# Performance work log

Measured on AMD Instinct MI355X. Metric: run time of the kernel, lower is better.

## Reference

```python
import jax, jax.numpy as jnp
import numpy as np

ALPHA = 0.9
T = 809          # doc_len_limit hard-coded in fofe_tricontext_encoder
M = 16           # opt['max_len'] (cand_len_limit)
BN_EPS = 1e-5


def _cand_indices(T, M):
    # Enumeration order matches get_sample_index: outer over start s, inner over span.
    s_list, e_list = [], []
    for s in range(T):
        for span in range(min(M, T - s)):
            s_list.append(s)
            e_list.append(s + span)
    return np.asarray(s_list, np.int32), np.asarray(e_list, np.int32)

_S_IDX, _E_IDX = _cand_indices(T, M)          # [N_CANDS] = [12824]
_SPAN = (_E_IDX - _S_IDX).astype(np.int64)
# FOFE decay coefficient alpha^(e-s+1) for subtracting the prefix before the span
_COEF = (ALPHA ** (_SPAN + 1)).astype(np.float32)
# Lower-triangular FOFE prefix operator: A[t,k] = alpha^(t-k) for k<=t
_DIFF = np.subtract.outer(np.arange(T), np.arange(T))
_AFWD = np.where(_DIFF >= 0, ALPHA ** np.maximum(_DIFF, 0), 0.0).astype(np.float32)


def _bn(x, g, b, m, v):
    return (x - m) * jax.lax.rsqrt(v + BN_EPS) * g + b


def _forward(doc_emb, query_emb, W1, g1, b1, m1, v1, W2, g2, b2, m2, v2, W3):
    B, Tt, Dd = doc_emb.shape
    A = jnp.asarray(_AFWD)
    # forward FOFE prefixes F[t] = sum_{k<=t} alpha^(t-k) x[k]; inverse FOFE suffixes
    F = jnp.einsum('tk,bkd->btd', A, doc_emb)          # [B,T,Dd]
    R = jnp.einsum('tk,bkd->btd', A.T, doc_emb)        # [B,T,Dd]
    Fp = jnp.concatenate([jnp.zeros((B, 1, Dd), F.dtype), F], axis=1)   # Fp[:,s]=F[s-1]
    Rp = jnp.concatenate([R, jnp.zeros((B, 1, Dd), R.dtype)], axis=1)   # Rp[:,e+1]
    s_idx = jnp.asarray(_S_IDX)
    e_idx = jnp.asarray(_E_IDX)
    coef = jnp.asarray(_COEF)
    lctx = Fp[:, s_idx]                                 # left context excl cand
    cand = F[:, e_idx] - coef[None, :, None] * Fp[:, s_idx]  # FOFE of span [s,e]
    rctx = Rp[:, e_idx + 1]                             # right context excl cand
    doc_fofe = jnp.concatenate([lctx, cand, rctx], axis=-1)  # [B,N,3*Dd]
    # query FOFE (fofe_linear): z = sum_t alpha^(Lq-1-t) q[t]
    Lq = query_emb.shape[1]
    w = (ALPHA ** jnp.arange(Lq - 1, -1, -1, dtype=jnp.float32))
    qf = jnp.einsum('t,btd->bd', w, query_emb)          # [B,E]
    N = doc_fofe.shape[1]
    qf_b = jnp.broadcast_to(qf[:, None, :], (B, N, qf.shape[-1]))
    dq = jnp.concatenate([doc_fofe, qf_b], axis=-1)     # [B,N,3*Dd+E]
    x = dq.reshape(B * N, -1)
    h = jax.nn.relu(_bn(x @ W1.T, g1, b1, m1, v1))      # 1x1 conv == GEMM
    h = jax.nn.relu(_bn(h @ W2.T, g2, b2, m2, v2))
    out = (h @ W3.T).reshape(B, N, 2)                   # 2 class scores per candidate
    return out


def setup_inputs() -> dict:
    key = jax.random.key(0)
    ks = jax.random.split(key, 13)
    B, Lq, Dd, E = 4, 30, 304, 300
    Cin, H4, H2 = 3 * Dd + E, 1024, 512
    return {
        'doc_emb': jax.random.normal(ks[0], (B, T, Dd), jnp.float32),
        'query_emb': jax.random.normal(ks[1], (B, Lq, E), jnp.float32),
        'W1': jax.random.normal(ks[2], (H4, Cin), jnp.float32) / np.sqrt(Cin),
        'g1': jax.random.normal(ks[3], (H4,), jnp.float32),
        'b1': jax.random.normal(ks[4], (H4,), jnp.float32),
        'm1': jax.random.normal(ks[5], (H4,), jnp.float32),
        'v1': jax.random.uniform(ks[6], (H4,), jnp.float32),
        'W2': jax.random.normal(ks[7], (H2, H4), jnp.float32) / np.sqrt(H4),
        'g2': jax.random.normal(ks[8], (H2,), jnp.float32),
        'b2': jax.random.normal(ks[9], (H2,), jnp.float32),
        'm2': jax.random.normal(ks[10], (H2,), jnp.float32),
        'v2': jax.random.uniform(ks[11], (H2,), jnp.float32),
        'W3': jax.random.normal(ks[12], (2, H2), jnp.float32) / np.sqrt(H2),
    }


def reference(doc_emb, query_emb, W1, g1, b1, m1, v1, W2, g2, b2, m2, v2, W3):
    return _forward(doc_emb, query_emb, W1, g1, b1, m1, v1, W2, g2, b2, m2, v2, W3)
```

## Files before the change

kernel.cpp:

```cpp
#include <hip/hip_runtime.h>
#include <string.h>

#define T_LEN   809
#define DD      304
#define EE      300
#define LQ      30
#define NCAND   12824
#define NPAD    12928
#define CIN     1212
#define H1      1024
#define H2      512
#define BATCH   4
#define MROWS_F (BATCH * NPAD)
#define KS      320
#define TPAD    3328
#define NROWS_U 3240

#define MP_SCAN0   0
#define MP_W1      416
#define MP_W2      4256
#define MP_BIAS2   6304
#define MP_BASE    6306
#define MP_RMAP    7330
#define MP_TOTAL   7532

__device__ __constant__ float c_coef[16] = {
  0.9f, 0.81f, 0.729f, 0.6561f, 0.59049f, 0.531441f, 0.4782969f, 0.43046721f,
  0.387420489f, 0.3486784401f, 0.31381059609f, 0.282429536481f,
  0.2541865828329f, 0.22876792454961f, 0.205891132094649f, 0.1853020188851841f
};

__device__ __forceinline__ unsigned short f2bf(float f) {
  unsigned int u = __float_as_uint(f);
  u += 0x7fffu + ((u >> 16) & 1u);
  return (unsigned short)(u >> 16);
}
__device__ __forceinline__ float bf2f(unsigned int h) {
  return __uint_as_float(h << 16);
}

typedef const __attribute__((address_space(1))) unsigned int GU32;
typedef __attribute__((address_space(3))) unsigned int LU32;
__device__ __forceinline__ void async16(const unsigned short* g, unsigned short* l) {
  __builtin_amdgcn_global_load_lds((GU32*)g, (LU32*)l, 16, 0, 0);
}

__device__ __forceinline__ unsigned int comb2(unsigned int ul, unsigned int uc,
                                              unsigned int ue, float cf) {
  float xlo = bf2f(ul & 0xffff) + bf2f(ue & 0xffff) - cf * bf2f(uc & 0xffff);
  float xhi = bf2f(ul >> 16)    + bf2f(ue >> 16)    - cf * bf2f(uc >> 16);
  xlo = xlo > 0.f ? xlo : 0.f;
  xhi = xhi > 0.f ? xhi : 0.f;
  return (unsigned int)f2bf(xlo) | ((unsigned int)f2bf(xhi) << 16);
}
__device__ __forceinline__ unsigned int add2(unsigned int a, unsigned int b) {
  const float lo = bf2f(a & 0xffff) + bf2f(b & 0xffff);
  const float hi = bf2f(a >> 16)    + bf2f(b >> 16);
  return (unsigned int)f2bf(lo) | ((unsigned int)f2bf(hi) << 16);
}

__global__ __launch_bounds__(256) void k_prep(const float* __restrict__ doc,
                                              const float* __restrict__ qe,
                                              const float* __restrict__ W1,
                                              const float* __restrict__ g1,
                                              const float* __restrict__ b1,
                                              const float* __restrict__ m1,
                                              const float* __restrict__ v1,
                                              const float* __restrict__ W2,
                                              const float* __restrict__ g2,
                                              const float* __restrict__ b2,
                                              const float* __restrict__ m2,
                                              const float* __restrict__ v2,
                                              unsigned short* __restrict__ Fz,
                                              unsigned short* __restrict__ Rz,
                                              unsigned short* __restrict__ Wlc,
                                              unsigned short* __restrict__ Wr,
                                              unsigned short* __restrict__ W2b,
                                              float* __restrict__ bias2,
                                              float* __restrict__ baseW,
                                              unsigned int* __restrict__ rowmap)
{
  __shared__ float qs[EE];
  const int vb  = blockIdx.x;
  const int tid = threadIdx.x;

  if (vb < MP_W1) {
    const int dchunk = vb & 1;
    const int rest   = vb >> 1;
    const int tchunk = rest % 26;
    const int b      = (rest / 26) & 3;
    const int dir    = rest / 104;
    const int d  = dchunk * 256 + tid;
    const int t0 = tchunk * 32;
    if (dir == 0) {
      if (tchunk == 0 && d < KS) Fz[((size_t)b * 810) * KS + d] = 0;
      if (d >= DD) return;
      const float* db = doc + (size_t)b * T_LEN * DD + d;
      int start = t0 - 96; if (start < 0) start = 0;
      int end = t0 + 31; if (end > T_LEN - 1) end = T_LEN - 1;
      float s = 0.f;
      for (int t = start; t <= end; ++t) {
        s = fmaf(0.9f, s, db[(size_t)t * DD]);
        if (t >= t0) Fz[((size_t)b * 810 + 1 + t) * KS + d] = f2bf(s);
      }
    } else {
      if (tchunk == 0 && d < KS) Rz[((size_t)b * 810 + 809) * KS + d] = 0;
      if (d >= DD) return;
      const float* db = doc + (size_t)b * T_LEN * DD + d;
      int t1 = t0 + 31; if (t1 > T_LEN - 1) t1 = T_LEN - 1;
      int start = t1 + 96; if (start > T_LEN - 1) start = T_LEN - 1;
      float s = 0.f;
      for (int t = start; t >= t0; --t) {
        s = fmaf(0.9f, s, db[(size_t)t * DD]);
        if (t <= t1) Rz[((size_t)b * 810 + t) * KS + d] = f2bf(s);
      }
    }
  } else if (vb < MP_W2) {
    const int e = (vb - MP_W1) * 256 + tid;
    const int j = e / KS;
    const int k = e - j * KS;
    int jj, koff; unsigned short* dst; size_t idx;
    if (j < 1024)      { jj = j;        koff = k;       dst = Wlc; idx = (size_t)j * KS + k; }
    else if (j < 2048) { jj = j - 1024; koff = 304 + k; dst = Wlc; idx = (size_t)j * KS + k; }
    else               { jj = j - 2048; koff = 608 + k; dst = Wr;  idx = (size_t)(j - 2048) * KS + k; }
    float w = 0.f;
    if (k < 304) w = W1[(size_t)jj * CIN + koff] * g1[jj] * rsqrtf(v1[jj] + 1e-5f);
    dst[idx] = f2bf(w);
  } else if (vb < MP_BIAS2) {
    const int e = (vb - MP_W2) * 256 + tid;
    const int j = e >> 10;
    const int k = e & 1023;
    const float w = W2[(size_t)j * H1 + k] * g2[j] * rsqrtf(v2[j] + 1e-5f);
    W2b[(size_t)j * H1 + k] = f2bf(w);
  } else if (vb < MP_BASE) {
    const int i = (vb - MP_BIAS2) * 256 + tid;
    if (i < H2) {
      const float s = g2[i] * rsqrtf(v2[i] + 1e-5f);
      bias2[i] = b2[i] - m2[i] * s;
    }
  } else if (vb < MP_RMAP) {
    const int flat = vb - MP_BASE;
    const int b  = flat >> 8;
    const int jg = flat & 255;
    const float* q = qe + (size_t)b * LQ * EE;
    for (int k = tid; k < EE; k += 256) {
      float s = 0.f;
      for (int t = 0; t < LQ; ++t) s = fmaf(s, 0.9f, q[(size_t)t * EE + k]);
      qs[k] = s;
    }
    __syncthreads();
    const int wv   = tid >> 6;
    const int lane = tid & 63;
    const int j = jg * 4 + wv;
    const float* w = W1 + (size_t)j * CIN + 912;
    float acc = 0.f;
    for (int k = lane; k < EE; k += 64) acc = fmaf(qs[k], w[k], acc);
    #pragma unroll
    for (int off = 32; off; off >>= 1) acc += __shfl_down(acc, off);
    if (lane == 0) {
      const float sc = g1[j] * rsqrtf(v1[j] + 1e-5f);
      baseW[(size_t)b * 2048 + j]        = b1[j] - m1[j] * sc + acc * sc;
      baseW[(size_t)b * 2048 + 1024 + j] = 0.f;
    }
  } else {
    const int g = (vb - MP_RMAP) * 256 + tid;
    const int b  = g / NPAD;
    const int rr = g - b * NPAD;
    unsigned int mv = 0;
    if (rr < NCAND) {
      int s, span;
      if (rr < 12704) { s = rr >> 4; span = rr & 15; }
      else {
        const int x = rr - 12704;
        int d = 0;
        while (d < 14 && x >= (15 * (d + 1) - ((d + 1) * d) / 2)) ++d;
        span = x - (15 * d - (d * (d - 1)) / 2);
        s = 794 + d;
      }
      const unsigned int srow = (unsigned int)(b * 810 + s);
      const unsigned int erow = (unsigned int)(b * 810 + s + span + 1);
      mv = srow | (erow << 12) | ((unsigned int)span << 24);
    }
    rowmap[g] = mv;
  }
}

typedef __attribute__((ext_vector_type(8))) short frag8;
typedef __attribute__((ext_vector_type(4))) float f32x4;

#define GEMM_KLOOP(A_, B_, K_)                                                   \
  __shared__ __align__(16) unsigned short As[128 * 32];                          \
  __shared__ __align__(16) unsigned short Bs[128 * 32];                          \
  const int tid  = threadIdx.x;                                                  \
  const int lane = tid & 63;                                                     \
  const int wv   = tid >> 6;                                                     \
  const int wm   = wv & 1, wn = wv >> 1;                                         \
  const int lr = lane >> 2;                                                      \
  const int lc = lane & 3;                                                       \
  const int sc = lc ^ ((lr >> 1) & 3);                                           \
  const unsigned short* gA = A_ + ((size_t)bm * 128 + wv * 32 + lr) * K_ + sc * 8; \
  const unsigned short* gB = B_ + ((size_t)bn * 128 + wv * 32 + lr) * K_ + sc * 8; \
  const size_t row16 = (size_t)16 * K_;                                          \
  unsigned short* lA0 = &As[wv * 1024];                                          \
  unsigned short* lB0 = &Bs[wv * 1024];                                          \
  f32x4 acc[4][4];                                                               \
  _Pragma("unroll")                                                              \
  for (int i = 0; i < 4; ++i)                                                    \
    _Pragma("unroll")                                                            \
    for (int j = 0; j < 4; ++j) acc[i][j] = (f32x4){0.f, 0.f, 0.f, 0.f};         \
  const int arow = lane & 15;                                                    \
  const int pg   = (lane >> 4) ^ ((arow >> 1) & 3);                              \
  const int aoff = (wm * 64 + arow) * 32 + pg * 8;                               \
  const int boff = (wn * 64 + arow) * 32 + pg * 8;                               \
  for (int kc = 0; kc < K_; kc += 32) {                                          \
    __syncthreads();                                                             \
    async16(gA + kc,         lA0);                                               \
    async16(gA + kc + row16, lA0 + 512);                                         \
    async16(gB + kc,         lB0);                                               \
    async16(gB + kc + row16, lB0 + 512);                                         \
    __syncthreads();                                                             \
    frag8 a[4], b[4];                                                            \
    _Pragma("unroll")                                                            \
    for (int i = 0; i < 4; ++i) a[i] = *(const frag8*)&As[aoff + i * 512];       \
    _Pragma("unroll")                                                            \
    for (int i = 0; i < 4; ++i) b[i] = *(const frag8*)&Bs[boff + i * 512];       \
    _Pragma("unroll")                                                            \
    for (int i = 0; i < 4; ++i)                                                  \
      _Pragma("unroll")                                                          \
      for (int j = 0; j < 4; ++j)                                                \
        acc[i][j] = __builtin_amdgcn_mfma_f32_16x16x32_bf16(a[i], b[j], acc[i][j], 0, 0, 0); \
  }

__global__ __launch_bounds__(256, 4) void k_ugemm(const unsigned short* __restrict__ Fz,
                                                  const unsigned short* __restrict__ Wlc,
                                                  const unsigned short* __restrict__ Rz,
                                                  const unsigned short* __restrict__ Wr,
                                                  const float* __restrict__ baseW,
                                                  unsigned short* __restrict__ UF,
                                                  unsigned short* __restrict__ UR)
{
  int bx = blockIdx.x;
  const int isUF = (bx < 416);
  const unsigned short *Ap, *Bp; unsigned short* Cp; int bn, bm, Nout;
  if (isUF) { Ap = Fz; Bp = Wlc; Cp = UF; bn = bx & 15; bm = bx >> 4; Nout = 2048; }
  else { bx -= 416; Ap = Rz; Bp = Wr; Cp = UR; bn = bx & 7; bm = bx >> 3; Nout = 1024; }
  GEMM_KLOOP(Ap, Bp, KS)
  const int crow0 = bm * 128 + wm * 64 + ((lane >> 4) << 2);
  const int ccol0 = bn * 128 + wn * 64 + arow;
  #pragma unroll
  for (int i = 0; i < 4; ++i)
    #pragma unroll
    for (int j = 0; j < 4; ++j) {
      const int col = ccol0 + j * 16;
      #pragma unroll
      for (int r = 0; r < 4; ++r) {
        const int row = crow0 + i * 16 + r;
        float v = acc[i][j][r];
        if (isUF) {
          int bb = row / 810; if (bb > 3) bb = 3;
          v += baseW[(size_t)bb * 2048 + col];
        }
        Cp[(size_t)row * Nout + col] = f2bf(v);
      }
    }
}

__global__ __launch_bounds__(256) void k_ucr(const unsigned short* __restrict__ UF,
                                             const unsigned short* __restrict__ UR,
                                             unsigned short* __restrict__ UCR)
{
  const int c = blockIdx.x * 256 + threadIdx.x;
  if (c >= NROWS_U * 128) return;
  const int t  = c >> 7;
  const int kk = (c & 127) * 8;
  const uint4 a = *(const uint4*)(UF + (size_t)t * 2048 + 1024 + kk);
  const uint4 b = *(const uint4*)(UR + (size_t)t * 1024 + kk);
  uint4 o;
  o.x = add2(a.x, b.x);
  o.y = add2(a.y, b.y);
  o.z = add2(a.z, b.z);
  o.w = add2(a.w, b.w);
  *(uint4*)(UCR + (size_t)t * 1024 + kk) = o;
}

__global__ __launch_bounds__(512, 2) void k_gemm2f(const unsigned short* __restrict__ UF,
                                                   const unsigned short* __restrict__ UCR,
                                                   const unsigned short* __restrict__ W2b,
                                                   const unsigned int* __restrict__ rowmap,
                                                   const float* __restrict__ bias,
                                                   const float* __restrict__ W3,
                                                   float* __restrict__ out)
{
  __shared__ __align__(16) unsigned short As[2 * 128 * 32];
  __shared__ __align__(16) unsigned short Bs[2 * 512 * 32];

  const int orig = blockIdx.x;
  const int xcd = orig & 7, cidx = orig >> 3;
  const int bm = (xcd < 4 ? xcd * 51 : 204 + (xcd - 4) * 50) + cidx;

  const int tid  = threadIdx.x;
  const int lane = tid & 63;
  const int w    = tid >> 6;
  const int wm   = w & 1;
  const int wn   = w >> 1;
  const int arow = lane & 15;
  const int lr   = lane >> 2;
  const int lc   = lane & 3;
  const int sc   = lc ^ ((lr >> 1) & 3);

  const int rA    = tid >> 2;
  const int cA    = tid & 3;
  const int physA = cA ^ ((rA >> 1) & 3);
  const unsigned int mv = rowmap[bm * 128 + rA];
  const float cf = c_coef[mv >> 24];
  const unsigned short* pUL = UF  + (size_t)(mv & 4095) * 2048 + cA * 8;
  const unsigned short* pUE = UCR + (size_t)((mv >> 12) & 4095) * 1024 + cA * 8;

  const unsigned short* gB = W2b + ((size_t)(w * 64 + lr)) * H1 + sc * 8;

  const int pg   = (lane >> 4) ^ ((arow >> 1) & 3);
  const int aoff = (wm * 64 + arow) * 32 + pg * 8;
  const int boff = (wn * 128 + arow) * 32 + pg * 8;

  f32x4 acc[4][8];
  #pragma unroll
  for (int i = 0; i < 4; ++i)
    #pragma unroll
    for (int j = 0; j < 8; ++j) acc[i][j] = (f32x4){0.f, 0.f, 0.f, 0.f};

  uint4 vulN = *(const uint4*)(pUL);
  uint4 vucN = *(const uint4*)(pUL + 1024);
  uint4 vueN = *(const uint4*)(pUE);
  {
    unsigned short* lB = &Bs[w * 2048];
    async16(gB,           lB);
    async16(gB + 16 * H1, lB + 512);
    async16(gB + 32 * H1, lB + 1024);
    async16(gB + 48 * H1, lB + 1536);
  }
  {
    uint4 o;
    o.x = comb2(vulN.x, vucN.x, vueN.x, cf);
    o.y = comb2(vulN.y, vucN.y, vueN.y, cf);
    o.z = comb2(vulN.z, vucN.z, vueN.z, cf);
    o.w = comb2(vulN.w, vucN.w, vueN.w, cf);
    *(uint4*)&As[rA * 32 + physA * 8] = o;
  }
  vulN = *(const uint4*)(pUL + 32);
  vucN = *(const uint4*)(pUL + 1024 + 32);
  vueN = *(const uint4*)(pUE + 32);
  asm volatile("s_waitcnt lgkmcnt(0)" ::: "memory");
  __builtin_amdgcn_sched_barrier(0);

  for (int k = 0; k < 32; ++k) {
    const int cur = k & 1, nxt = cur ^ 1;
    __builtin_amdgcn_s_barrier();
    __builtin_amdgcn_sched_barrier(0);
    if (k < 31) {
      const int kn = (k + 1) * 32;
      unsigned short* lB = &Bs[nxt * 16384 + w * 2048];
      async16(gB + kn,           lB);
      async16(gB + kn + 16 * H1, lB + 512);
      async16(gB + kn + 32 * H1, lB + 1024);
      async16(gB + kn + 48 * H1, lB + 1536);
      __builtin_amdgcn_sched_barrier(0);
      asm volatile("s_waitcnt vmcnt(4)" ::: "memory");
      __builtin_amdgcn_sched_barrier(0);
      uint4 o;
      o.x = comb2(vulN.x, vucN.x, vueN.x, cf);
      o.y = comb2(vulN.y, vucN.y, vueN.y, cf);
      o.z = comb2(vulN.z, vucN.z, vueN.z, cf);
      o.w = comb2(vulN.w, vucN.w, vueN.w, cf);
      *(uint4*)&As[nxt * 4096 + rA * 32 + physA * 8] = o;
      if (k < 30) {
        const int kg = (k + 2) * 32;
        vulN = *(const uint4*)(pUL + kg);
        vucN = *(const uint4*)(pUL + 1024 + kg);
        vueN = *(const uint4*)(pUE + kg);
      }
    } else {
      __builtin_amdgcn_sched_barrier(0);
      asm volatile("s_waitcnt vmcnt(0)" ::: "memory");
      __builtin_amdgcn_sched_barrier(0);
    }
    __builtin_amdgcn_sched_barrier(0);
    frag8 a[4], b[8];
    #pragma unroll
    for (int i = 0; i < 4; ++i) a[i] = *(const frag8*)&As[cur * 4096 + aoff + i * 512];
    #pragma unroll
    for (int j = 0; j < 8; ++j) b[j] = *(const frag8*)&Bs[cur * 16384 + boff + j * 512];
    __builtin_amdgcn_s_setprio(1);
    #pragma unroll
    for (int i = 0; i < 4; ++i)
      #pragma unroll
      for (int j = 0; j < 8; ++j)
        acc[i][j] = __builtin_amdgcn_mfma_f32_16x16x32_bf16(a[i], b[j], acc[i][j], 0, 0, 0);
    __builtin_amdgcn_s_setprio(0);
  }

  __syncthreads();
  float* redf = (float*)As;

  float bj[8], w0v[8], w1v[8];
  #pragma unroll
  for (int j = 0; j < 8; ++j) {
    const int col = wn * 128 + j * 16 + arow;
    bj[j]  = bias[col];
    w0v[j] = W3[col];
    w1v[j] = W3[H2 + col];
  }
  const int grp = lane >> 4;
  #pragma unroll
  for (int i = 0; i < 4; ++i)
    #pragma unroll
    for (int r = 0; r < 4; ++r) {
      float q0 = 0.f, q1 = 0.f;
      #pragma unroll
      for (int j = 0; j < 8; ++j) {
        float v = acc[i][j][r] + bj[j];
        v = v > 0.f ? v : 0.f;
        q0 = fmaf(v, w0v[j], q0);
        q1 = fmaf(v, w1v[j], q1);
      }
      #pragma unroll
      for (int m = 1; m < 16; m <<= 1) { q0 += __shfl_xor(q0, m); q1 += __shfl_xor(q1, m); }
      if (arow == 0) {
        const int rl = wm * 64 + i * 16 + grp * 4 + r;
        redf[rl * 8 + wn * 2 + 0] = q0;
        redf[rl * 8 + wn * 2 + 1] = q1;
      }
    }
  __syncthreads();
  if (tid < 256) {
    const int rl = tid >> 1, s = tid & 1;
    const float v = redf[rl * 8 + 0 + s] + redf[rl * 8 + 2 + s]
                  + redf[rl * 8 + 4 + s] + redf[rl * 8 + 6 + s];
    const int row = bm * 128 + rl;
    const int b   = row / NPAD;
    const int rr  = row - b * NPAD;
    if (rr < NCAND) out[((size_t)b * NCAND + rr) * 2 + s] = v;
  }
}

extern "C" void kernel_launch(void* const* d_in, const int* in_sizes, int n_in,
                              void* d_out, int out_size, void* d_ws, size_t ws_size,
                              hipStream_t stream)
{
  const float* doc = (const float*)d_in[0];
  const float* qe  = (const float*)d_in[1];
  const float* W1  = (const float*)d_in[2];
  const float* g1  = (const float*)d_in[3];
  const float* b1  = (const float*)d_in[4];
  const float* m1  = (const float*)d_in[5];
  const float* v1  = (const float*)d_in[6];
  const float* W2  = (const float*)d_in[7];
  const float* g2  = (const float*)d_in[8];
  const float* b2  = (const float*)d_in[9];
  const float* m2  = (const float*)d_in[10];
  const float* v2  = (const float*)d_in[11];
  const float* W3  = (const float*)d_in[12];
  float* out = (float*)d_out;

  char* ws = (char*)d_ws;
  size_t off = 0;
  auto alloc = [&](size_t bytes) -> void* {
    void* p = ws + off;
    off = (off + bytes + 255) & ~(size_t)255;
    return p;
  };
  unsigned short* Fz    = (unsigned short*)alloc((size_t)TPAD * KS * 2);
  unsigned short* Rz    = (unsigned short*)alloc((size_t)TPAD * KS * 2);
  unsigned short* Wlc   = (unsigned short*)alloc((size_t)2048 * KS * 2);
  unsigned short* Wr    = (unsigned short*)alloc((size_t)1024 * KS * 2);
  unsigned short* W2b   = (unsigned short*)alloc((size_t)H2 * H1 * 2);
  float*          bias2 = (float*)alloc((size_t)H2 * 4);
  float*          baseW = (float*)alloc((size_t)BATCH * 2048 * 4);
  unsigned short* UF    = (unsigned short*)alloc((size_t)TPAD * 2048 * 2);
  unsigned short* UR    = (unsigned short*)alloc((size_t)TPAD * 1024 * 2);
  unsigned short* UCR   = (unsigned short*)alloc((size_t)NROWS_U * 1024 * 2);
  unsigned int*   rowmap= (unsigned int*)alloc((size_t)MROWS_F * 4);
  (void)ws_size;

  k_prep<<<dim3(MP_TOTAL), 256, 0, stream>>>(doc, qe, W1, g1, b1, m1, v1,
                                             W2, g2, b2, m2, v2,
                                             Fz, Rz, Wlc, Wr, W2b, bias2, baseW, rowmap);
  k_ugemm<<<dim3(416 + 208), 256, 0, stream>>>(Fz, Wlc, Rz, Wr, baseW, UF, UR);
  k_ucr<<<dim3((NROWS_U * 128 + 255) / 256), 256, 0, stream>>>(UF, UR, UCR);
  k_gemm2f<<<dim3(404), 512, 0, stream>>>(UF, UCR, W2b, rowmap, bias2, W3, out);
}
```

Measured before the change: 234.1 us.

## Split gemm2 N dimension across two blocks with partial-sum finalize kernel

The fused second GEMM now splits the 512 output columns into two 256-wide halves. This doubles the grid to 808 blocks, halves the per-block B tile and accumulators, and raises launch bounds to allow 4 blocks per CU. Each half writes partial W3 projections to a workspace buffer, and a new small kernel sums the two halves into the output. The aim is better occupancy and load balance across CUs. The cost is that the A-tile gather and combine work is done twice, plus an extra launch and a partial-sum round trip through memory.

New measurement: 226.1 us. 1.04x faster.

```diff
diff --git a/kernel.cpp b/kernel.cpp
--- a/kernel.cpp
+++ b/kernel.cpp
@@ -283,20 +283,20 @@
   *(uint4*)(UCR + (size_t)t * 1024 + kk) = o;
 }
 
-__global__ __launch_bounds__(512, 2) void k_gemm2f(const unsigned short* __restrict__ UF,
+__global__ __launch_bounds__(512, 4) void k_gemm2f(const unsigned short* __restrict__ UF,
                                                    const unsigned short* __restrict__ UCR,
                                                    const unsigned short* __restrict__ W2b,
                                                    const unsigned int* __restrict__ rowmap,
                                                    const float* __restrict__ bias,
                                                    const float* __restrict__ W3,
-                                                   float* __restrict__ out)
+                                                   float* __restrict__ P)
 {
   __shared__ __align__(16) unsigned short As[2 * 128 * 32];
-  __shared__ __align__(16) unsigned short Bs[2 * 512 * 32];
+  __shared__ __align__(16) unsigned short Bs[2 * 256 * 32];
 
   const int orig = blockIdx.x;
-  const int xcd = orig & 7, cidx = orig >> 3;
-  const int bm = (xcd < 4 ? xcd * 51 : 204 + (xcd - 4) * 50) + cidx;
+  const int wg = (orig & 7) * 101 + (orig >> 3);
+  const int bm = wg >> 1, bn = wg & 1;
 
   const int tid  = threadIdx.x;
   const int lane = tid & 63;
@@ -316,27 +316,25 @@
   const unsigned short* pUL = UF  + (size_t)(mv & 4095) * 2048 + cA * 8;
   const unsigned short* pUE = UCR + (size_t)((mv >> 12) & 4095) * 1024 + cA * 8;
 
-  const unsigned short* gB = W2b + ((size_t)(w * 64 + lr)) * H1 + sc * 8;
+  const unsigned short* gB = W2b + ((size_t)(bn * 256 + w * 32 + lr)) * H1 + sc * 8;
 
   const int pg   = (lane >> 4) ^ ((arow >> 1) & 3);
   const int aoff = (wm * 64 + arow) * 32 + pg * 8;
-  const int boff = (wn * 128 + arow) * 32 + pg * 8;
-
-  f32x4 acc[4][8];
+  const int boff = (wn * 64 + arow) * 32 + pg * 8;
+
+  f32x4 acc[4][4];
   #pragma unroll
   for (int i = 0; i < 4; ++i)
     #pragma unroll
-    for (int j = 0; j < 8; ++j) acc[i][j] = (f32x4){0.f, 0.f, 0.f, 0.f};
+    for (int j = 0; j < 4; ++j) acc[i][j] = (f32x4){0.f, 0.f, 0.f, 0.f};
 
   uint4 vulN = *(const uint4*)(pUL);
   uint4 vucN = *(const uint4*)(pUL + 1024);
   uint4 vueN = *(const uint4*)(pUE);
   {
-    unsigned short* lB = &Bs[w * 2048];
+    unsigned short* lB = &Bs[w * 1024];
     async16(gB,           lB);
     async16(gB + 16 * H1, lB + 512);
-    async16(gB + 32 * H1, lB + 1024);
-    async16(gB + 48 * H1, lB + 1536);
   }
   {
     uint4 o;
@@ -349,7 +347,7 @@
   vulN = *(const uint4*)(pUL + 32);
   vucN = *(const uint4*)(pUL + 1024 + 32);
   vueN = *(const uint4*)(pUE + 32);
-  asm volatile("s_waitcnt lgkmcnt(0)" ::: "memory");
+  asm volatile("s_waitcnt vmcnt(3) lgkmcnt(0)" ::: "memory");
   __builtin_amdgcn_sched_barrier(0);
 
   for (int k = 0; k < 32; ++k) {
@@ -358,13 +356,11 @@
     __builtin_amdgcn_sched_barrier(0);
     if (k < 31) {
       const int kn = (k + 1) * 32;
-      unsigned short* lB = &Bs[nxt * 16384 + w * 2048];
+      unsigned short* lB = &Bs[nxt * 8192 + w * 1024];
       async16(gB + kn,           lB);
       async16(gB + kn + 16 * H1, lB + 512);
-      async16(gB + kn + 32 * H1, lB + 1024);
-      async16(gB + kn + 48 * H1, lB + 1536);
       __builtin_amdgcn_sched_barrier(0);
-      asm volatile("s_waitcnt vmcnt(4)" ::: "memory");
+      asm volatile("s_waitcnt vmcnt(2)" ::: "memory");
       __builtin_amdgcn_sched_barrier(0);
       uint4 o;
       o.x = comb2(vulN.x, vucN.x, vueN.x, cf);
@@ -378,33 +374,33 @@
         vucN = *(const uint4*)(pUL + 1024 + kg);
         vueN = *(const uint4*)(pUE + kg);
       }
-    } else {
-      __builtin_amdgcn_sched_barrier(0);
-      asm volatile("s_waitcnt vmcnt(0)" ::: "memory");
-      __builtin_amdgcn_sched_barrier(0);
     }
     __builtin_amdgcn_sched_barrier(0);
-    frag8 a[4], b[8];
+    frag8 a[4], b[4];
     #pragma unroll
     for (int i = 0; i < 4; ++i) a[i] = *(const frag8*)&As[cur * 4096 + aoff + i * 512];
     #pragma unroll
-    for (int j = 0; j < 8; ++j) b[j] = *(const frag8*)&Bs[cur * 16384 + boff + j * 512];
+    for (int j = 0; j < 4; ++j) b[j] = *(const frag8*)&Bs[cur * 8192 + boff + j * 512];
     __builtin_amdgcn_s_setprio(1);
     #pragma unroll
     for (int i = 0; i < 4; ++i)
       #pragma unroll
-      for (int j = 0; j < 8; ++j)
+      for (int j = 0; j < 4; ++j)
         acc[i][j] = __builtin_amdgcn_mfma_f32_16x16x32_bf16(a[i], b[j], acc[i][j], 0, 0, 0);
     __builtin_amdgcn_s_setprio(0);
+    __builtin_amdgcn_sched_barrier(0);
+    if (k < 30)       { asm volatile("s_waitcnt vmcnt(3)" ::: "memory"); }
+    else if (k == 30) { asm volatile("s_waitcnt vmcnt(0)" ::: "memory"); }
+    __builtin_amdgcn_sched_barrier(0);
   }
 
   __syncthreads();
   float* redf = (float*)As;
 
-  float bj[8], w0v[8], w1v[8];
+  float bj[4], w0v[4], w1v[4];
   #pragma unroll
-  for (int j = 0; j < 8; ++j) {
-    const int col = wn * 128 + j * 16 + arow;
+  for (int j = 0; j < 4; ++j) {
+    const int col = bn * 256 + wn * 64 + j * 16 + arow;
     bj[j]  = bias[col];
     w0v[j] = W3[col];
     w1v[j] = W3[H2 + col];
@@ -416,7 +412,7 @@
     for (int r = 0; r < 4; ++r) {
       float q0 = 0.f, q1 = 0.f;
       #pragma unroll
-      for (int j = 0; j < 8; ++j) {
+      for (int j = 0; j < 4; ++j) {
         float v = acc[i][j][r] + bj[j];
         v = v > 0.f ? v : 0.f;
         q0 = fmaf(v, w0v[j], q0);
@@ -426,20 +422,30 @@
       for (int m = 1; m < 16; m <<= 1) { q0 += __shfl_xor(q0, m); q1 += __shfl_xor(q1, m); }
       if (arow == 0) {
         const int rl = wm * 64 + i * 16 + grp * 4 + r;
-        redf[rl * 8 + wn * 2 + 0] = q0;
-        redf[rl * 8 + wn * 2 + 1] = q1;
+        redf[(rl * 4 + wn) * 2]     = q0;
+        redf[(rl * 4 + wn) * 2 + 1] = q1;
       }
     }
   __syncthreads();
   if (tid < 256) {
     const int rl = tid >> 1, s = tid & 1;
-    const float v = redf[rl * 8 + 0 + s] + redf[rl * 8 + 2 + s]
-                  + redf[rl * 8 + 4 + s] + redf[rl * 8 + 6 + s];
-    const int row = bm * 128 + rl;
-    const int b   = row / NPAD;
-    const int rr  = row - b * NPAD;
-    if (rr < NCAND) out[((size_t)b * NCAND + rr) * 2 + s] = v;
-  }
+    const float v = redf[(rl * 4 + 0) * 2 + s] + redf[(rl * 4 + 1) * 2 + s]
+                  + redf[(rl * 4 + 2) * 2 + s] + redf[(rl * 4 + 3) * 2 + s];
+    P[((size_t)(bm * 128 + rl)) * 4 + bn * 2 + s] = v;
+  }
+}
+
+__global__ __launch_bounds__(256) void k_fin(const float* __restrict__ P, float* __restrict__ out)
+{
+  const int row = blockIdx.x * 256 + threadIdx.x;
+  if (row >= MROWS_F) return;
+  const int b = row / NPAD;
+  const int rr = row - b * NPAD;
+  if (rr >= NCAND) return;
+  const float4 pa = ((const float4*)P)[row];
+  float* o = out + ((size_t)b * NCAND + rr) * 2;
+  o[0] = pa.x + pa.z;
+  o[1] = pa.y + pa.w;
 }
 
 extern "C" void kernel_launch(void* const* d_in, const int* in_sizes, int n_in,
@@ -479,6 +485,7 @@
   unsigned short* UR    = (unsigned short*)alloc((size_t)TPAD * 1024 * 2);
   unsigned short* UCR   = (unsigned short*)alloc((size_t)NROWS_U * 1024 * 2);
   unsigned int*   rowmap= (unsigned int*)alloc((size_t)MROWS_F * 4);
+  float*          P     = (float*)alloc((size_t)MROWS_F * 4 * 4);
   (void)ws_size;
 
   k_prep<<<dim3(MP_TOTAL), 256, 0, stream>>>(doc, qe, W1, g1, b1, m1, v1,
@@ -486,5 +493,6 @@
                                              Fz, Rz, Wlc, Wr, W2b, bias2, baseW, rowmap);
   k_ugemm<<<dim3(416 + 208), 256, 0, stream>>>(Fz, Wlc, Rz, Wr, baseW, UF, UR);
   k_ucr<<<dim3((NROWS_U * 128 + 255) / 256), 256, 0, stream>>>(UF, UR, UCR);
-  k_gemm2f<<<dim3(404), 512, 0, stream>>>(UF, UCR, W2b, rowmap, bias2, W3, out);
-}
+  k_gemm2f<<<dim3(808), 512, 0, stream>>>(UF, UCR, W2b, rowmap, bias2, W3, P);
+  k_fin<<<dim3((MROWS_F + 255) / 256), 256, 0, stream>>>(P, out);
+}
```
